# Kernel optimization log

Hardware: AMD Instinct MI355X
Metric: run time of the kernel (lower is better)

The kernel has to match this reference:

```python
import jax, jax.numpy as jnp
import numpy as np

B, S, H, D = 8, 1024, 1024, 64

def setup_inputs() -> dict:
    key = jax.random.key(0)
    ks = jax.random.split(key, 8)
    return {
        "query": jax.random.normal(ks[0], (B, S, H), jnp.float32),
        "key": jax.random.normal(ks[1], (B, S, H), jnp.float32),
        "value": jax.random.normal(ks[2], (B, S, H), jnp.float32),
        "Wq": jax.random.normal(ks[3], (H, D), jnp.float32) * 0.02,
        "bq": jnp.zeros((D,), jnp.float32),
        "Wk": jax.random.normal(ks[4], (H, D), jnp.float32) * 0.02,
        "bk": jnp.zeros((D,), jnp.float32),
        "Wv": jax.random.normal(ks[5], (H, D), jnp.float32) * 0.02,
        "bv": jnp.zeros((D,), jnp.float32),
        "k_bias_matrix": jax.random.normal(ks[6], (S, S, D), jnp.float32) * 0.02,
        "v_bias_matrix": jax.random.normal(ks[7], (S, S, D), jnp.float32) * 0.02,
        "mask": jnp.ones((B, S), jnp.int32),
    }

def reference(query, key, value, Wq, bq, Wk, bk, Wv, bv, k_bias_matrix, v_bias_matrix, mask):
    # Linear projections: [B,S,H] -> [B,S,D]
    q = query @ Wq + bq
    k = key @ Wk + bk
    v = value @ Wv + bv
    # Standard content score + Shaw relative-position key bias score
    attn_1 = jnp.einsum('bqd,bkd->bqk', q, k)
    attn_2 = jnp.einsum('bqd,qkd->bqk', q, k_bias_matrix)
    scores = (attn_1 + attn_2) / jnp.sqrt(jnp.float32(D))
    scores = jnp.where(mask[:, None, :] == 0, jnp.float32(-1e9), scores)
    w = jax.nn.softmax(scores, axis=-1)  # [B,S,S]
    values_1 = jnp.einsum('bqk,bkd->bqd', w, v)
    values_2 = jnp.einsum('bqk,qkd->bqd', w, v_bias_matrix)
    return values_1 + values_2
```

## Files before the change

kernel.cpp:

```cpp
#include <hip/hip_runtime.h>
#include <hip/hip_bf16.h>
#include <cstdint>
#include <cstddef>

#define NB 8
#define NS 1024
#define NH 1024
#define ND 64

typedef __attribute__((ext_vector_type(8))) short bf8_t;
typedef __attribute__((ext_vector_type(4))) float f32x4;
typedef __attribute__((ext_vector_type(4))) short short4v;

__device__ __forceinline__ short f2bfs(float x) {
    union { __hip_bfloat16 h; short s; } u;
    u.h = __float2bfloat16(x);
    return u.s;
}
__device__ __forceinline__ float bf2f(unsigned short h) {
    return __uint_as_float(((unsigned int)h) << 16);
}
__device__ __forceinline__ bf8_t pack_bf8(float4 a, float4 b) {
    bf8_t r;
    r[0] = f2bfs(a.x); r[1] = f2bfs(a.y); r[2] = f2bfs(a.z); r[3] = f2bfs(a.w);
    r[4] = f2bfs(b.x); r[5] = f2bfs(b.y); r[6] = f2bfs(b.z); r[7] = f2bfs(b.w);
    return r;
}

#define QP_OFF  0
#define KP_OFF  524288
#define VPT_OFF 1048576
#define S1_OFF  1572864
#define S2_OFF  9961472

__global__ __launch_bounds__(256, 2) void proj_kernel(
    const float* __restrict__ qin, const float* __restrict__ kin, const float* __restrict__ vin,
    const float* __restrict__ Wq, const float* __restrict__ bq,
    const float* __restrict__ Wk, const float* __restrict__ bk,
    const float* __restrict__ Wv, const float* __restrict__ bv,
    short* __restrict__ ws_s)
{
    __shared__ short Wt[64][136];

    const int p = blockIdx.y;
    const float* A    = (p == 0) ? qin : (p == 1) ? kin : vin;
    const float* W    = (p == 0) ? Wq  : (p == 1) ? Wk  : Wv;
    const float* bias = (p == 0) ? bq  : (p == 1) ? bk  : bv;

    const int t  = threadIdx.x;
    const int wv = t >> 6, l = t & 63, lr = l & 15, lg = l >> 4;
    const int rw = blockIdx.x * 64 + wv * 16;

    const int sk  = t & 127;
    const int snh = (t >> 7) * 32;

    f32x4 acc[4];
    #pragma unroll
    for (int n = 0; n < 4; ++n) acc[n] = (f32x4){0.f, 0.f, 0.f, 0.f};

    for (int ch = 0; ch < 8; ++ch) {
        __syncthreads();
        {
            const float* wp = &W[(size_t)(ch * 128 + sk) * ND + snh];
            #pragma unroll
            for (int j = 0; j < 8; ++j) {
                float4 w4 = *(const float4*)&wp[4 * j];
                Wt[snh + 4 * j + 0][sk] = f2bfs(w4.x);
                Wt[snh + 4 * j + 1][sk] = f2bfs(w4.y);
                Wt[snh + 4 * j + 2][sk] = f2bfs(w4.z);
                Wt[snh + 4 * j + 3][sk] = f2bfs(w4.w);
            }
        }
        __syncthreads();
        #pragma unroll
        for (int s = 0; s < 4; ++s) {
            const float* ap = &A[(size_t)(rw + lr) * NH + ch * 128 + s * 32 + lg * 8];
            bf8_t af = pack_bf8(*(const float4*)ap, *(const float4*)(ap + 4));
            #pragma unroll
            for (int n = 0; n < 4; ++n) {
                bf8_t bf = *(const bf8_t*)&Wt[n * 16 + lr][s * 32 + lg * 8];
                acc[n] = __builtin_amdgcn_mfma_f32_16x16x32_bf16(af, bf, acc[n], 0, 0, 0);
            }
        }
    }

    if (p < 2) {
        short* dst = ws_s + ((p == 0) ? QP_OFF : KP_OFF);
        const float sc = (p == 0) ? 0.125f : 1.0f;
        #pragma unroll
        for (int n = 0; n < 4; ++n) {
            const float bs = bias[n * 16 + lr];
            #pragma unroll
            for (int r = 0; r < 4; ++r)
                dst[(size_t)(rw + lg * 4 + r) * ND + n * 16 + lr] = f2bfs((acc[n][r] + bs) * sc);
        }
    } else {
        short* vpT = ws_s + VPT_OFF;
        const int b = rw >> 10;
        const int sbase = (rw & 1023) + lg * 4;
        #pragma unroll
        for (int n = 0; n < 4; ++n) {
            const float bs = bias[n * 16 + lr];
            short4v pk;
            #pragma unroll
            for (int r = 0; r < 4; ++r) pk[r] = f2bfs(acc[n][r] + bs);
            *(short4v*)&vpT[((size_t)b * 64 + n * 16 + lr) * NS + sbase] = pk;
        }
    }
}

__global__ __launch_bounds__(256, 4) void scores_kernel(
    const short* __restrict__ ws_s,
    const float* __restrict__ kbias,
    short* __restrict__ s1, short* __restrict__ s2)
{
    const short* qp = ws_s + QP_OFF;
    const short* kp = ws_s + KP_OFF;
    const int t = threadIdx.x;
    const int wv = t >> 6, l = t & 63, lr = l & 15, lg = l >> 4;
    const int q0 = blockIdx.y * 16;
    const int k0 = blockIdx.x * 64 + wv * 16;

    #pragma unroll
    for (int b = 0; b < 8; ++b) {
        const short* ap = &qp[((size_t)b * NS + q0 + lr) * ND + lg * 8];
        const short* bp = &kp[((size_t)b * NS + k0 + lr) * ND + lg * 8];
        bf8_t a0 = *(const bf8_t*)ap;
        bf8_t a1 = *(const bf8_t*)(ap + 32);
        bf8_t b0 = *(const bf8_t*)bp;
        bf8_t b1 = *(const bf8_t*)(bp + 32);
        f32x4 acc = {0.f, 0.f, 0.f, 0.f};
        acc = __builtin_amdgcn_mfma_f32_16x16x32_bf16(a0, b0, acc, 0, 0, 0);
        acc = __builtin_amdgcn_mfma_f32_16x16x32_bf16(a1, b1, acc, 0, 0, 0);
        #pragma unroll
        for (int r = 0; r < 4; ++r)
            s1[((size_t)b * NS + q0 + lg * 4 + r) * NS + k0 + lr] = f2bfs(acc[r]);
    }

    #pragma unroll 4
    for (int qq = 0; qq < 16; ++qq) {
        const short* ap = &qp[((size_t)(lr & 7) * NS + q0 + qq) * ND + lg * 8];
        bf8_t a0 = *(const bf8_t*)ap;
        bf8_t a1 = *(const bf8_t*)(ap + 32);
        const float* kb = &kbias[((size_t)(q0 + qq) * NS + k0 + lr) * ND + lg * 8];
        bf8_t b0 = pack_bf8(*(const float4*)kb, *(const float4*)(kb + 4));
        bf8_t b1 = pack_bf8(*(const float4*)(kb + 32), *(const float4*)(kb + 36));
        f32x4 acc = {0.f, 0.f, 0.f, 0.f};
        acc = __builtin_amdgcn_mfma_f32_16x16x32_bf16(a0, b0, acc, 0, 0, 0);
        acc = __builtin_amdgcn_mfma_f32_16x16x32_bf16(a1, b1, acc, 0, 0, 0);
        if (lg < 2) {
            #pragma unroll
            for (int r = 0; r < 4; ++r)
                s2[((size_t)(q0 + qq) * NB + lg * 4 + r) * NS + k0 + lr] = f2bfs(acc[r]);
        }
    }
}

__global__ __launch_bounds__(256, 4) void softmax_kernel(
    short* __restrict__ s1, const short* __restrict__ s2,
    const int* __restrict__ mask)
{
    const int t = threadIdx.x, wv = t >> 6, l = t & 63;
    const int row = blockIdx.x * 4 + wv;
    const int b = row >> 10, q = row & 1023;
    short* r1 = s1 + (size_t)row * NS;
    const short* r2 = s2 + ((size_t)q * NB + b) * NS;
    const int* mb = mask + b * NS;
    const float LOG2E = 1.4426950408889634f;
    const int k0 = l * 16;

    unsigned short sa[16], sb[16];
    *(uint4*)&sa[0] = *(const uint4*)&r1[k0];
    *(uint4*)&sa[8] = *(const uint4*)&r1[k0 + 8];
    *(uint4*)&sb[0] = *(const uint4*)&r2[k0];
    *(uint4*)&sb[8] = *(const uint4*)&r2[k0 + 8];
    int mv[16];
    #pragma unroll
    for (int j = 0; j < 4; ++j) *(int4*)&mv[4 * j] = *(const int4*)&mb[k0 + 4 * j];

    float x[16];
    float m = -3.0e38f;
    #pragma unroll
    for (int j = 0; j < 16; ++j) {
        float v = bf2f(sa[j]) + bf2f(sb[j]);
        if (mv[j] == 0) v = -1e9f;
        x[j] = v;
        m = fmaxf(m, v);
    }
    #pragma unroll
    for (int off = 1; off < 64; off <<= 1) m = fmaxf(m, __shfl_xor(m, off, 64));

    float lsum = 0.f;
    #pragma unroll
    for (int j = 0; j < 16; ++j) { x[j] = exp2f((x[j] - m) * LOG2E); lsum += x[j]; }
    #pragma unroll
    for (int off = 1; off < 64; off <<= 1) lsum += __shfl_xor(lsum, off, 64);
    const float il = 1.0f / fmaxf(lsum, 1e-30f);

    #pragma unroll
    for (int j = 0; j < 16; ++j) sa[j] = (unsigned short)f2bfs(x[j] * il);
    *(uint4*)&r1[k0]     = *(const uint4*)&sa[0];
    *(uint4*)&r1[k0 + 8] = *(const uint4*)&sa[8];
}

__global__ __launch_bounds__(256, 2) void v1_kernel(
    const short* __restrict__ ws_s, const short* __restrict__ w,
    float* __restrict__ out)
{
    const short* vpT = ws_s + VPT_OFF;
    const int t = threadIdx.x, wv = t >> 6, l = t & 63, lr = l & 15, lg = l >> 4;
    const int b = blockIdx.y;
    const int q0 = blockIdx.x * 16;

    f32x4 acc[4];
    #pragma unroll
    for (int j = 0; j < 4; ++j) acc[j] = (f32x4){0.f, 0.f, 0.f, 0.f};

    const short* arow = &w[((size_t)b * NS + q0 + lr) * NS + lg * 8];
    const short* brow = &vpT[((size_t)b * ND + wv * 16 + lr) * NS + lg * 8];
    #pragma unroll 8
    for (int ch = 0; ch < 32; ++ch) {
        bf8_t a  = *(const bf8_t*)(arow + ch * 32);
        bf8_t bb = *(const bf8_t*)(brow + ch * 32);
        acc[ch & 3] = __builtin_amdgcn_mfma_f32_16x16x32_bf16(a, bb, acc[ch & 3], 0, 0, 0);
    }
    f32x4 s;
    #pragma unroll
    for (int r = 0; r < 4; ++r) s[r] = acc[0][r] + acc[1][r] + acc[2][r] + acc[3][r];

    #pragma unroll
    for (int r = 0; r < 4; ++r)
        out[((size_t)b * NS + q0 + lg * 4 + r) * ND + wv * 16 + lr] = s[r];
}

__global__ __launch_bounds__(256, 4) void outv2_kernel(
    const short* __restrict__ w,
    const float* __restrict__ vbias,
    float* __restrict__ out)
{
    __shared__ short Wl[8][1024];
    __shared__ float otile[4][8][64];

    const int t = threadIdx.x, wv = t >> 6, l = t & 63;
    const int q = blockIdx.x;

    {
        const int rr = t >> 5;
        const int c0 = (t & 31) * 32;
        const short* src = &w[((size_t)rr * NS + q) * NS + c0];
        #pragma unroll
        for (int j = 0; j < 4; ++j)
            *(uint4*)&Wl[rr][c0 + j * 8] = *(const uint4*)&src[j * 8];
    }
    __syncthreads();

    const int kq = l >> 4;
    const int dq = l & 15;
    const int kw = wv * 256;
    const float* vbq = vbias + (size_t)q * NS * ND;

    float4 av[8];
    #pragma unroll
    for (int b = 0; b < 8; ++b) av[b] = make_float4(0.f, 0.f, 0.f, 0.f);

    #pragma unroll 4
    for (int i = 0; i < 64; ++i) {
        const int k = kw + kq + 4 * i;
        const float4 vb = *(const float4*)&vbq[(size_t)k * ND + 4 * dq];
        #pragma unroll
        for (int b = 0; b < 8; ++b) {
            const float wgt = bf2f((unsigned short)Wl[b][k]);
            av[b].x += wgt * vb.x; av[b].y += wgt * vb.y;
            av[b].z += wgt * vb.z; av[b].w += wgt * vb.w;
        }
    }
    #pragma unroll
    for (int b = 0; b < 8; ++b) {
        #pragma unroll
        for (int off = 16; off <= 32; off <<= 1) {
            av[b].x += __shfl_xor(av[b].x, off, 64);
            av[b].y += __shfl_xor(av[b].y, off, 64);
            av[b].z += __shfl_xor(av[b].z, off, 64);
            av[b].w += __shfl_xor(av[b].w, off, 64);
        }
    }
    if (l < 16) {
        #pragma unroll
        for (int b = 0; b < 8; ++b)
            *(float4*)&otile[wv][b][4 * l] = av[b];
    }
    __syncthreads();

    if (t < 128) {
        const int b = t >> 4, dd = (t & 15) * 4;
        float4 s0 = *(const float4*)&otile[0][b][dd];
        float4 s1v = *(const float4*)&otile[1][b][dd];
        float4 s2v = *(const float4*)&otile[2][b][dd];
        float4 s3v = *(const float4*)&otile[3][b][dd];
        float* op = &out[((size_t)b * NS + q) * ND + dd];
        float4 pv = *(const float4*)op;
        float4 o;
        o.x = pv.x + s0.x + s1v.x + s2v.x + s3v.x;
        o.y = pv.y + s0.y + s1v.y + s2v.y + s3v.y;
        o.z = pv.z + s0.z + s1v.z + s2v.z + s3v.z;
        o.w = pv.w + s0.w + s1v.w + s2v.w + s3v.w;
        *(float4*)op = o;
    }
}

extern "C" void kernel_launch(void* const* d_in, const int* in_sizes, int n_in,
                              void* d_out, int out_size, void* d_ws, size_t ws_size,
                              hipStream_t stream) {
    (void)in_sizes; (void)n_in; (void)out_size; (void)ws_size;
    const float* query = (const float*)d_in[0];
    const float* key   = (const float*)d_in[1];
    const float* value = (const float*)d_in[2];
    const float* Wq    = (const float*)d_in[3];
    const float* bq    = (const float*)d_in[4];
    const float* Wk    = (const float*)d_in[5];
    const float* bk    = (const float*)d_in[6];
    const float* Wv    = (const float*)d_in[7];
    const float* bv    = (const float*)d_in[8];
    const float* kbias = (const float*)d_in[9];
    const float* vbias = (const float*)d_in[10];
    const int*   mask  = (const int*)d_in[11];
    short* ws_s = (short*)d_ws;
    short* s1 = ws_s + S1_OFF;
    short* s2 = ws_s + S2_OFF;
    float* outp = (float*)d_out;

    proj_kernel<<<dim3(128, 3), 256, 0, stream>>>(query, key, value, Wq, bq, Wk, bk, Wv, bv, ws_s);
    scores_kernel<<<dim3(16, 64), 256, 0, stream>>>(ws_s, kbias, s1, s2);
    softmax_kernel<<<2048, 256, 0, stream>>>(s1, s2, mask);
    v1_kernel<<<dim3(64, 8), 256, 0, stream>>>(ws_s, s1, outp);
    outv2_kernel<<<1024, 256, 0, stream>>>(s1, vbias, outp);
}
```

Before: 207.2 us.

## Fuse relative-bias scores, softmax and value-bias output into one per-query kernel

```diff
diff --git a/kernel.cpp b/kernel.cpp
--- a/kernel.cpp
+++ b/kernel.cpp
@@ -31,7 +31,6 @@
 #define KP_OFF  524288
 #define VPT_OFF 1048576
 #define S1_OFF  1572864
-#define S2_OFF  9961472
 
 __global__ __launch_bounds__(256, 2) void proj_kernel(
     const float* __restrict__ qin, const float* __restrict__ kin, const float* __restrict__ vin,
@@ -40,7 +39,7 @@
     const float* __restrict__ Wv, const float* __restrict__ bv,
     short* __restrict__ ws_s)
 {
-    __shared__ short Wt[64][136];
+    __shared__ short Wt[2][64][136];
 
     const int p = blockIdx.y;
     const float* A    = (p == 0) ? qin : (p == 1) ? kin : vin;
@@ -58,30 +57,43 @@
     #pragma unroll
     for (int n = 0; n < 4; ++n) acc[n] = (f32x4){0.f, 0.f, 0.f, 0.f};
 
+    {
+        const float* wp = &W[(size_t)sk * ND + snh];
+        #pragma unroll
+        for (int j = 0; j < 8; ++j) {
+            float4 w4 = *(const float4*)&wp[4 * j];
+            Wt[0][snh + 4 * j + 0][sk] = f2bfs(w4.x);
+            Wt[0][snh + 4 * j + 1][sk] = f2bfs(w4.y);
+            Wt[0][snh + 4 * j + 2][sk] = f2bfs(w4.z);
+            Wt[0][snh + 4 * j + 3][sk] = f2bfs(w4.w);
+        }
+    }
+    __syncthreads();
+
     for (int ch = 0; ch < 8; ++ch) {
-        __syncthreads();
-        {
-            const float* wp = &W[(size_t)(ch * 128 + sk) * ND + snh];
+        const int cur = ch & 1;
+        if (ch < 7) {
+            const float* wp = &W[(size_t)((ch + 1) * 128 + sk) * ND + snh];
             #pragma unroll
             for (int j = 0; j < 8; ++j) {
                 float4 w4 = *(const float4*)&wp[4 * j];
-                Wt[snh + 4 * j + 0][sk] = f2bfs(w4.x);
-                Wt[snh + 4 * j + 1][sk] = f2bfs(w4.y);
-                Wt[snh + 4 * j + 2][sk] = f2bfs(w4.z);
-                Wt[snh + 4 * j + 3][sk] = f2bfs(w4.w);
-            }
-        }
-        __syncthreads();
+                Wt[cur ^ 1][snh + 4 * j + 0][sk] = f2bfs(w4.x);
+                Wt[cur ^ 1][snh + 4 * j + 1][sk] = f2bfs(w4.y);
+                Wt[cur ^ 1][snh + 4 * j + 2][sk] = f2bfs(w4.z);
+                Wt[cur ^ 1][snh + 4 * j + 3][sk] = f2bfs(w4.w);
+            }
+        }
         #pragma unroll
         for (int s = 0; s < 4; ++s) {
             const float* ap = &A[(size_t)(rw + lr) * NH + ch * 128 + s * 32 + lg * 8];
             bf8_t af = pack_bf8(*(const float4*)ap, *(const float4*)(ap + 4));
             #pragma unroll
             for (int n = 0; n < 4; ++n) {
-                bf8_t bf = *(const bf8_t*)&Wt[n * 16 + lr][s * 32 + lg * 8];
+                bf8_t bf = *(const bf8_t*)&Wt[cur][n * 16 + lr][s * 32 + lg * 8];
                 acc[n] = __builtin_amdgcn_mfma_f32_16x16x32_bf16(af, bf, acc[n], 0, 0, 0);
             }
         }
+        __syncthreads();
     }
 
     if (p < 2) {
@@ -109,10 +121,8 @@
     }
 }
 
-__global__ __launch_bounds__(256, 4) void scores_kernel(
-    const short* __restrict__ ws_s,
-    const float* __restrict__ kbias,
-    short* __restrict__ s1, short* __restrict__ s2)
+__global__ __launch_bounds__(256, 4) void scores_c_kernel(
+    const short* __restrict__ ws_s, short* __restrict__ s1)
 {
     const short* qp = ws_s + QP_OFF;
     const short* kp = ws_s + KP_OFF;
@@ -136,71 +146,144 @@
         for (int r = 0; r < 4; ++r)
             s1[((size_t)b * NS + q0 + lg * 4 + r) * NS + k0 + lr] = f2bfs(acc[r]);
     }
-
-    #pragma unroll 4
-    for (int qq = 0; qq < 16; ++qq) {
-        const short* ap = &qp[((size_t)(lr & 7) * NS + q0 + qq) * ND + lg * 8];
-        bf8_t a0 = *(const bf8_t*)ap;
-        bf8_t a1 = *(const bf8_t*)(ap + 32);
-        const float* kb = &kbias[((size_t)(q0 + qq) * NS + k0 + lr) * ND + lg * 8];
-        bf8_t b0 = pack_bf8(*(const float4*)kb, *(const float4*)(kb + 4));
-        bf8_t b1 = pack_bf8(*(const float4*)(kb + 32), *(const float4*)(kb + 36));
-        f32x4 acc = {0.f, 0.f, 0.f, 0.f};
-        acc = __builtin_amdgcn_mfma_f32_16x16x32_bf16(a0, b0, acc, 0, 0, 0);
-        acc = __builtin_amdgcn_mfma_f32_16x16x32_bf16(a1, b1, acc, 0, 0, 0);
-        if (lg < 2) {
-            #pragma unroll
-            for (int r = 0; r < 4; ++r)
-                s2[((size_t)(q0 + qq) * NB + lg * 4 + r) * NS + k0 + lr] = f2bfs(acc[r]);
-        }
-    }
-}
-
-__global__ __launch_bounds__(256, 4) void softmax_kernel(
-    short* __restrict__ s1, const short* __restrict__ s2,
-    const int* __restrict__ mask)
+}
+
+__global__ __launch_bounds__(256, 4) void mega_kernel(
+    const short* __restrict__ ws_s,
+    short* __restrict__ s1,
+    const float* __restrict__ kbias,
+    const float* __restrict__ vbias,
+    const int* __restrict__ mask,
+    float* __restrict__ out)
 {
-    const int t = threadIdx.x, wv = t >> 6, l = t & 63;
-    const int row = blockIdx.x * 4 + wv;
-    const int b = row >> 10, q = row & 1023;
-    short* r1 = s1 + (size_t)row * NS;
-    const short* r2 = s2 + ((size_t)q * NB + b) * NS;
-    const int* mb = mask + b * NS;
-    const float LOG2E = 1.4426950408889634f;
-    const int k0 = l * 16;
-
-    unsigned short sa[16], sb[16];
-    *(uint4*)&sa[0] = *(const uint4*)&r1[k0];
-    *(uint4*)&sa[8] = *(const uint4*)&r1[k0 + 8];
-    *(uint4*)&sb[0] = *(const uint4*)&r2[k0];
-    *(uint4*)&sb[8] = *(const uint4*)&r2[k0 + 8];
-    int mv[16];
-    #pragma unroll
-    for (int j = 0; j < 4; ++j) *(int4*)&mv[4 * j] = *(const int4*)&mb[k0 + 4 * j];
-
-    float x[16];
-    float m = -3.0e38f;
-    #pragma unroll
-    for (int j = 0; j < 16; ++j) {
-        float v = bf2f(sa[j]) + bf2f(sb[j]);
-        if (mv[j] == 0) v = -1e9f;
-        x[j] = v;
-        m = fmaxf(m, v);
-    }
-    #pragma unroll
-    for (int off = 1; off < 64; off <<= 1) m = fmaxf(m, __shfl_xor(m, off, 64));
-
-    float lsum = 0.f;
-    #pragma unroll
-    for (int j = 0; j < 16; ++j) { x[j] = exp2f((x[j] - m) * LOG2E); lsum += x[j]; }
-    #pragma unroll
-    for (int off = 1; off < 64; off <<= 1) lsum += __shfl_xor(lsum, off, 64);
-    const float il = 1.0f / fmaxf(lsum, 1e-30f);
-
-    #pragma unroll
-    for (int j = 0; j < 16; ++j) sa[j] = (unsigned short)f2bfs(x[j] * il);
-    *(uint4*)&r1[k0]     = *(const uint4*)&sa[0];
-    *(uint4*)&r1[k0 + 8] = *(const uint4*)&sa[8];
+    __shared__ short Wt[8][1024];
+    __shared__ short Sb[8][1032];
+
+    const short* qp = ws_s + QP_OFF;
+    const int q = blockIdx.x, t = threadIdx.x;
+    const int wv = t >> 6, l = t & 63, lr = l & 15, lg = l >> 4;
+
+    {
+        const bf8_t aq0 = *(const bf8_t*)&qp[((size_t)(lr & 7) * NS + q) * ND + lg * 8];
+        const bf8_t aq1 = *(const bf8_t*)&qp[((size_t)(lr & 7) * NS + q) * ND + 32 + lg * 8];
+        const float* kbq = kbias + (size_t)q * NS * ND;
+
+        #pragma unroll 4
+        for (int it = 0; it < 16; ++it) {
+            const int k0 = wv * 256 + it * 16;
+            const float* kb = &kbq[(size_t)(k0 + lr) * ND + lg * 8];
+            bf8_t b0 = pack_bf8(*(const float4*)kb, *(const float4*)(kb + 4));
+            bf8_t b1 = pack_bf8(*(const float4*)(kb + 32), *(const float4*)(kb + 36));
+            f32x4 acc = {0.f, 0.f, 0.f, 0.f};
+            acc = __builtin_amdgcn_mfma_f32_16x16x32_bf16(aq0, b0, acc, 0, 0, 0);
+            acc = __builtin_amdgcn_mfma_f32_16x16x32_bf16(aq1, b1, acc, 0, 0, 0);
+            if (lg < 2) {
+                #pragma unroll
+                for (int r = 0; r < 4; ++r)
+                    Sb[lg * 4 + r][k0 + lr] = f2bfs(acc[r]);
+            }
+        }
+    }
+    __syncthreads();
+
+    {
+        const int b = t >> 5, idx = t & 31;
+        const int kk = idx * 32;
+        short* r1 = s1 + ((size_t)b * NS + q) * NS + kk;
+        const int* mb = mask + b * NS + kk;
+        const float LOG2E = 1.4426950408889634f;
+
+        float x[32];
+        float m = -3.0e38f;
+        #pragma unroll
+        for (int c = 0; c < 4; ++c) {
+            uint4 a4 = *(const uint4*)&r1[8 * c];
+            uint4 b4 = *(const uint4*)&Sb[b][kk + 8 * c];
+            int4 m0 = *(const int4*)&mb[8 * c];
+            int4 m1 = *(const int4*)&mb[8 * c + 4];
+            const unsigned short* ap = (const unsigned short*)&a4;
+            const unsigned short* bp = (const unsigned short*)&b4;
+            const int* mp = (const int*)&m0;
+            const int* mq = (const int*)&m1;
+            #pragma unroll
+            for (int j = 0; j < 8; ++j) {
+                float v = bf2f(ap[j]) + bf2f(bp[j]);
+                const int mvv = (j < 4) ? mp[j] : mq[j - 4];
+                v = (mvv == 0) ? -1e9f : v;
+                x[8 * c + j] = v;
+                m = fmaxf(m, v);
+            }
+        }
+        #pragma unroll
+        for (int off = 1; off < 32; off <<= 1) m = fmaxf(m, __shfl_xor(m, off, 32));
+
+        float lsum = 0.f;
+        #pragma unroll
+        for (int j = 0; j < 32; ++j) { x[j] = exp2f((x[j] - m) * LOG2E); lsum += x[j]; }
+        #pragma unroll
+        for (int off = 1; off < 32; off <<= 1) lsum += __shfl_xor(lsum, off, 32);
+        const float il = 1.0f / fmaxf(lsum, 1e-30f);
+
+        unsigned short wv16[32];
+        #pragma unroll
+        for (int j = 0; j < 32; ++j) wv16[j] = (unsigned short)f2bfs(x[j] * il);
+        #pragma unroll
+        for (int c = 0; c < 4; ++c) {
+            *(uint4*)&Wt[b][kk + 8 * c] = *(const uint4*)&wv16[8 * c];
+            *(uint4*)&r1[8 * c]         = *(const uint4*)&wv16[8 * c];
+        }
+    }
+    __syncthreads();
+
+    float* otile = (float*)&Sb[0][0];
+    {
+        const int kq = l >> 4, dq = l & 15;
+        const int kw = wv * 256;
+        const float* vbq = vbias + (size_t)q * NS * ND;
+
+        float4 av[8];
+        #pragma unroll
+        for (int b = 0; b < 8; ++b) av[b] = make_float4(0.f, 0.f, 0.f, 0.f);
+
+        #pragma unroll 4
+        for (int i = 0; i < 64; ++i) {
+            const int k = kw + kq + 4 * i;
+            const float4 vb = *(const float4*)&vbq[(size_t)k * ND + 4 * dq];
+            #pragma unroll
+            for (int b = 0; b < 8; ++b) {
+                const float wgt = bf2f((unsigned short)Wt[b][k]);
+                av[b].x += wgt * vb.x; av[b].y += wgt * vb.y;
+                av[b].z += wgt * vb.z; av[b].w += wgt * vb.w;
+            }
+        }
+        #pragma unroll
+        for (int b = 0; b < 8; ++b) {
+            #pragma unroll
+            for (int off = 16; off <= 32; off <<= 1) {
+                av[b].x += __shfl_xor(av[b].x, off, 64);
+                av[b].y += __shfl_xor(av[b].y, off, 64);
+                av[b].z += __shfl_xor(av[b].z, off, 64);
+                av[b].w += __shfl_xor(av[b].w, off, 64);
+            }
+        }
+        if (l < 16) {
+            #pragma unroll
+            for (int b = 0; b < 8; ++b)
+                *(float4*)&otile[((size_t)wv * 8 + b) * 64 + 4 * l] = av[b];
+        }
+    }
+    __syncthreads();
+
+    if (t < 128) {
+        const int b = t >> 4, dd = (t & 15) * 4;
+        float4 s = make_float4(0.f, 0.f, 0.f, 0.f);
+        #pragma unroll
+        for (int w4 = 0; w4 < 4; ++w4) {
+            float4 r = *(const float4*)&otile[((size_t)w4 * 8 + b) * 64 + dd];
+            s.x += r.x; s.y += r.y; s.z += r.z; s.w += r.w;
+        }
+        *(float4*)&out[((size_t)b * NS + q) * ND + dd] = s;
+    }
 }
 
 __global__ __launch_bounds__(256, 2) void v1_kernel(
@@ -229,82 +312,9 @@
     for (int r = 0; r < 4; ++r) s[r] = acc[0][r] + acc[1][r] + acc[2][r] + acc[3][r];
 
     #pragma unroll
-    for (int r = 0; r < 4; ++r)
-        out[((size_t)b * NS + q0 + lg * 4 + r) * ND + wv * 16 + lr] = s[r];
-}
-
-__global__ __launch_bounds__(256, 4) void outv2_kernel(
-    const short* __restrict__ w,
-    const float* __restrict__ vbias,
-    float* __restrict__ out)
-{
-    __shared__ short Wl[8][1024];
-    __shared__ float otile[4][8][64];
-
-    const int t = threadIdx.x, wv = t >> 6, l = t & 63;
-    const int q = blockIdx.x;
-
-    {
-        const int rr = t >> 5;
-        const int c0 = (t & 31) * 32;
-        const short* src = &w[((size_t)rr * NS + q) * NS + c0];
-        #pragma unroll
-        for (int j = 0; j < 4; ++j)
-            *(uint4*)&Wl[rr][c0 + j * 8] = *(const uint4*)&src[j * 8];
-    }
-    __syncthreads();
-
-    const int kq = l >> 4;
-    const int dq = l & 15;
-    const int kw = wv * 256;
-    const float* vbq = vbias + (size_t)q * NS * ND;
-
-    float4 av[8];
-    #pragma unroll
-    for (int b = 0; b < 8; ++b) av[b] = make_float4(0.f, 0.f, 0.f, 0.f);
-
-    #pragma unroll 4
-    for (int i = 0; i < 64; ++i) {
-        const int k = kw + kq + 4 * i;
-        const float4 vb = *(const float4*)&vbq[(size_t)k * ND + 4 * dq];
-        #pragma unroll
-        for (int b = 0; b < 8; ++b) {
-            const float wgt = bf2f((unsigned short)Wl[b][k]);
-            av[b].x += wgt * vb.x; av[b].y += wgt * vb.y;
-            av[b].z += wgt * vb.z; av[b].w += wgt * vb.w;
-        }
-    }
-    #pragma unroll
-    for (int b = 0; b < 8; ++b) {
-        #pragma unroll
-        for (int off = 16; off <= 32; off <<= 1) {
-            av[b].x += __shfl_xor(av[b].x, off, 64);
-            av[b].y += __shfl_xor(av[b].y, off, 64);
-            av[b].z += __shfl_xor(av[b].z, off, 64);
-            av[b].w += __shfl_xor(av[b].w, off, 64);
-        }
-    }
-    if (l < 16) {
-        #pragma unroll
-        for (int b = 0; b < 8; ++b)
-            *(float4*)&otile[wv][b][4 * l] = av[b];
-    }
-    __syncthreads();
-
-    if (t < 128) {
-        const int b = t >> 4, dd = (t & 15) * 4;
-        float4 s0 = *(const float4*)&otile[0][b][dd];
-        float4 s1v = *(const float4*)&otile[1][b][dd];
-        float4 s2v = *(const float4*)&otile[2][b][dd];
-        float4 s3v = *(const float4*)&otile[3][b][dd];
-        float* op = &out[((size_t)b * NS + q) * ND + dd];
-        float4 pv = *(const float4*)op;
-        float4 o;
-        o.x = pv.x + s0.x + s1v.x + s2v.x + s3v.x;
-        o.y = pv.y + s0.y + s1v.y + s2v.y + s3v.y;
-        o.z = pv.z + s0.z + s1v.z + s2v.z + s3v.z;
-        o.w = pv.w + s0.w + s1v.w + s2v.w + s3v.w;
-        *(float4*)op = o;
+    for (int r = 0; r < 4; ++r) {
+        float* op = &out[((size_t)b * NS + q0 + lg * 4 + r) * ND + wv * 16 + lr];
+        *op = *op + s[r];
     }
 }
 
@@ -326,12 +336,10 @@
     const int*   mask  = (const int*)d_in[11];
     short* ws_s = (short*)d_ws;
     short* s1 = ws_s + S1_OFF;
-    short* s2 = ws_s + S2_OFF;
     float* outp = (float*)d_out;
 
     proj_kernel<<<dim3(128, 3), 256, 0, stream>>>(query, key, value, Wq, bq, Wk, bk, Wv, bv, ws_s);
-    scores_kernel<<<dim3(16, 64), 256, 0, stream>>>(ws_s, kbias, s1, s2);
-    softmax_kernel<<<2048, 256, 0, stream>>>(s1, s2, mask);
+    scores_c_kernel<<<dim3(16, 64), 256, 0, stream>>>(ws_s, s1);
+    mega_kernel<<<1024, 256, 0, stream>>>(ws_s, s1, kbias, vbias, mask, outp);
     v1_kernel<<<dim3(64, 8), 256, 0, stream>>>(ws_s, s1, outp);
-    outv2_kernel<<<1024, 256, 0, stream>>>(s1, vbias, outp);
-}
+}
```

Result: faster. 191.1 us (-7.8%).
